# Performance work log

Measured on AMD Instinct MI355X. Metric: run time of the kernel, lower is better.

The kernel has to match this reference:

```python
import jax, jax.numpy as jnp
import numpy as np

C = 256
H = 8
D = C // H
B = 8
Q_PER = 128
KV_PER = 1024
NQ = B * Q_PER
NKV = B * KV_PER
NEG = -10000.0
MASK_EPS = 1e-6
RMS_EPS = float(np.finfo(np.float32).eps)  # torch RMSNorm default eps=None -> finfo eps


def _rms(x, w):
    return x * jax.lax.rsqrt(jnp.mean(x * x, axis=-1, keepdims=True) + RMS_EPS) * w


def _mlp(x, w1, b1, w2, b2):
    h = jax.nn.gelu(x @ w1.T + b1, approximate=False)  # torch nn.GELU is exact
    return h @ w2.T + b2


def _sdpa(qh, kh, vh, mask, scale):
    # qh [H, Nq, D], kh/vh [H, Nk, D], mask [Nq, Nk] additive
    s = jnp.einsum('hqd,hkd->hqk', qh, kh) * scale + mask[None]
    return jnp.einsum('hqk,hkd->hqd', jax.nn.softmax(s, axis=-1), vh)


def _heads(x):
    return x.reshape(-1, H, D).transpose(1, 0, 2)  # [H, N, D]


def setup_inputs() -> dict:
    key = jax.random.key(0)
    ks = jax.random.split(key, 24)
    s = 0.02
    lin = lambda k, o, i: jax.random.normal(k, (o, i), jnp.float32) * s
    inp = {
        'q': jax.random.normal(ks[0], (NQ, C), jnp.float32),
        'kv': jax.random.normal(ks[1], (NKV, C), jnp.float32),
        'cu_seqlens_q': jnp.arange(B + 1, dtype=jnp.int32) * Q_PER,
        'cu_seqlens_kv': jnp.arange(B + 1, dtype=jnp.int32) * KV_PER,
        'w_norm_kv': jnp.ones((C,), jnp.float32),
        'w_norm1': jnp.ones((C,), jnp.float32),
        'w_norm2': jnp.ones((C,), jnp.float32),
        'w_norm3': jnp.ones((C,), jnp.float32),
        'wq_c': lin(ks[2], C, C), 'wk_c': lin(ks[3], C, C), 'wv_c': lin(ks[4], C, C),
        'wo_c': lin(ks[5], C, C), 'bo_c': jnp.zeros((C,), jnp.float32),
        'wq_s': lin(ks[6], C, C), 'wkv_s': lin(ks[7], 2 * C, C),
        'wo_s': lin(ks[8], C, C), 'bo_s': jnp.zeros((C,), jnp.float32),
        'w1_mlp': lin(ks[9], 4 * C, C), 'b1_mlp': jnp.zeros((4 * C,), jnp.float32),
        'w2_mlp': lin(ks[10], C, 4 * C), 'b2_mlp': jnp.zeros((C,), jnp.float32),
        'w1_mask': lin(ks[11], C, C), 'b1_mask': jnp.zeros((C,), jnp.float32),
        'w2_mask': lin(ks[12], C, C), 'b2_mask': jnp.zeros((C,), jnp.float32),
    }
    return inp


def reference(q, kv, cu_seqlens_q, cu_seqlens_kv, w_norm_kv, w_norm1, w_norm2, w_norm3,
              wq_c, wk_c, wv_c, wo_c, bo_c, wq_s, wkv_s, wo_s, bo_s,
              w1_mlp, b1_mlp, w2_mlp, b2_mlp, w1_mask, b1_mask, w2_mask, b2_mask):
    scale = D ** (-0.5)
    nq, nkv = q.shape[0], kv.shape[0]
    # segment id per packed token from cu_seqlens
    seg_q = jnp.searchsorted(cu_seqlens_q, jnp.arange(nq), side='right') - 1
    seg_kv = jnp.searchsorted(cu_seqlens_kv, jnp.arange(nkv), side='right') - 1

    kv_n = _rms(kv, w_norm_kv)

    # mask MLP -> predicted attention mask (logits z), detached log-prob mask
    m_k = _mlp(q, w1_mask, b1_mask, w2_mask, b2_mask)          # [Nq, C]
    z = m_k @ kv_n.T                                           # [Nq, Nkv]
    p_hat = jax.nn.sigmoid(z)
    same = seg_q[:, None] == seg_kv[None, :]
    attn_mask = jnp.where(same, jnp.log(jax.lax.stop_gradient(p_hat) + MASK_EPS), NEG)

    # cross-attention (pre-norm)
    q_n = _rms(q, w_norm1)
    feat = _sdpa(_heads(q_n @ wq_c.T), _heads(kv_n @ wk_c.T), _heads(kv_n @ wv_c.T),
                 attn_mask, scale)
    feat = feat.transpose(1, 0, 2).reshape(-1, C) @ wo_c.T + bo_c
    q = q + feat

    # block-diagonal self-attention over queries
    q_n = _rms(q, w_norm2)
    kv_proj = (q_n @ wkv_s.T).reshape(-1, 2, H, D)
    self_mask = jnp.where(seg_q[:, None] == seg_q[None, :], 0.0, NEG)
    feat = _sdpa(_heads(q_n @ wq_s.T),
                 kv_proj[:, 0].transpose(1, 0, 2), kv_proj[:, 1].transpose(1, 0, 2),
                 self_mask, scale)
    feat = feat.transpose(1, 0, 2).reshape(-1, C) @ wo_s.T + bo_s
    q = q + feat

    # MLP
    q = q + _mlp(_rms(q, w_norm3), w1_mlp, b1_mlp, w2_mlp, b2_mlp)
    return q
```

## Files before the change

kernel.cpp:

```cpp
#include <hip/hip_runtime.h>
#include <math.h>


#define SCALE_ATTN 0.17677669529663687f
#define RMS_EPS 1.1920929e-07f

typedef __attribute__((ext_vector_type(8))) short bh8;
typedef __attribute__((ext_vector_type(4))) float f32x4;

__device__ __forceinline__ float bf2f(unsigned short s) {
  union { float f; unsigned u; } v; v.u = ((unsigned)s) << 16; return v.f;
}
__device__ __forceinline__ unsigned short f2bf(float f) {
  union { float f; unsigned u; } v; v.f = f;
  unsigned r = v.u + 0x7FFFu + ((v.u >> 16) & 1u);
  return (unsigned short)(r >> 16);
}
__device__ __forceinline__ unsigned pack2bf(float a, float b) {
  union { float f; unsigned u; } x, y; x.f = a; y.f = b;
  return ((x.u + 0x8000u) >> 16) | ((y.u + 0x8000u) & 0xFFFF0000u);
}
__device__ __forceinline__ float gelu_exact(float x) {
  return 0.5f * x * (1.0f + erff(x * 0.70710678118654752440f));
}
__device__ __forceinline__ float sum8sq(int4 v) {
  float s = 0.f;
  unsigned u[4] = {(unsigned)v.x, (unsigned)v.y, (unsigned)v.z, (unsigned)v.w};
#pragma unroll
  for (int i = 0; i < 4; ++i) {
    union { float f; unsigned q; } lo, hi;
    lo.q = u[i] << 16;
    hi.q = u[i] & 0xFFFF0000u;
    s += lo.f * lo.f + hi.f * hi.f;
  }
  return s;
}

struct WP { const float* p[12]; };
__global__ __launch_bounds__(256) void k_pre(
    WP wp, unsigned short* __restrict__ wbf, unsigned short* __restrict__ w2t,
    const float* __restrict__ wn1, const float* __restrict__ wn2,
    const float* __restrict__ wn3,
    const float* __restrict__ kv, const float* __restrict__ wnkv,
    const float* __restrict__ b2m, unsigned short* __restrict__ kv_n,
    float* __restrict__ tvec, unsigned short* __restrict__ q_n) {
  int bid = blockIdx.x, tid = threadIdx.x;
  if (bid < 1408) {
    long g = ((long)bid * 256 + tid) * 4;
    const float* src; long l;
    if (g < 327680)       { src = wp.p[g >> 16]; l = g & 65535; }
    else if (g < 458752)  { src = wp.p[5];  l = g - 327680; }
    else if (g < 524288)  { src = wp.p[6];  l = g - 458752; }
    else if (g < 786432)  { src = wp.p[7];  l = g - 524288; }
    else if (g < 1048576) { src = wp.p[8];  l = g - 786432; }
    else if (g < 1114112) { src = wp.p[9];  l = g - 1048576; }
    else if (g < 1179648) { src = wp.p[10]; l = g - 1114112; }
    else                  { src = wp.p[11]; l = g - 1179648; }
    float4 v = *(const float4*)(src + l);
    if (g >= 262144 && g < 458752) {
      int k = (int)(g & 255);
      v.x *= wn2[k]; v.y *= wn2[k + 1]; v.z *= wn2[k + 2]; v.w *= wn2[k + 3];
    } else if (g >= 524288 && g < 786432) {
      int k = (int)(g & 255);
      v.x *= wn3[k]; v.y *= wn3[k + 1]; v.z *= wn3[k + 2]; v.w *= wn3[k + 3];
    }
    ushort4 o;
    o.x = f2bf(v.x); o.y = f2bf(v.y); o.z = f2bf(v.z); o.w = f2bf(v.w);
    *(ushort4*)(wbf + g) = o;
  } else if (bid < 1424) {
    __shared__ float Ts[64][65];
    int t = bid - 1408, ti = t >> 2, tj = t & 3;
    const float* w2src = wp.p[10];
    int rr = tid >> 2;
#pragma unroll
    for (int j = 0; j < 4; ++j) {
      int cc = (tid & 3) * 16 + j * 4;
      float4 v = *(const float4*)(w2src + (long)(ti * 64 + rr) * 256 + tj * 64 + cc);
      Ts[rr][cc] = v.x; Ts[rr][cc + 1] = v.y;
      Ts[rr][cc + 2] = v.z; Ts[rr][cc + 3] = v.w;
    }
    __syncthreads();
#pragma unroll
    for (int j = 0; j < 4; ++j) {
      int kk = (tid & 3) * 16 + j * 4;
      ushort4 o;
      o.x = f2bf(Ts[kk][rr]); o.y = f2bf(Ts[kk + 1][rr]);
      o.z = f2bf(Ts[kk + 2][rr]); o.w = f2bf(Ts[kk + 3][rr]);
      *(ushort4*)(w2t + (long)(tj * 64 + rr) * 256 + ti * 64 + kk) = o;
    }
  } else if (bid < 3472) {
    int row = (bid - 1424) * 4 + (tid >> 6);
    int c4 = (tid & 63) * 4;
    float4 v = *(const float4*)(kv + (long)row * 256 + c4);
    float s = v.x * v.x + v.y * v.y + v.z * v.z + v.w * v.w;
#pragma unroll
    for (int off = 32; off > 0; off >>= 1) s += __shfl_xor(s, off, 64);
    float inv = rsqrtf(s * (1.0f / 256.0f) + RMS_EPS);
    float4 wn = *(const float4*)(wnkv + c4);
    float4 b2 = *(const float4*)(b2m + c4);
    float4 vn;
    vn.x = v.x * inv * wn.x; vn.y = v.y * inv * wn.y;
    vn.z = v.z * inv * wn.z; vn.w = v.w * inv * wn.w;
    ushort4 o;
    o.x = f2bf(vn.x); o.y = f2bf(vn.y); o.z = f2bf(vn.z); o.w = f2bf(vn.w);
    *(ushort4*)(kv_n + (long)row * 256 + c4) = o;
    float s2 = vn.x * b2.x + vn.y * b2.y + vn.z * b2.z + vn.w * b2.w;
#pragma unroll
    for (int off = 32; off > 0; off >>= 1) s2 += __shfl_xor(s2, off, 64);
    if ((tid & 63) == 0) tvec[row] = s2;
  } else {
    int row = (bid - 3472) * 4 + (tid >> 6);
    int c4 = (tid & 63) * 4;
    const float* q = wp.p[11];
    float4 v = *(const float4*)(q + (long)row * 256 + c4);
    float s = v.x * v.x + v.y * v.y + v.z * v.z + v.w * v.w;
#pragma unroll
    for (int off = 32; off > 0; off >>= 1) s += __shfl_xor(s, off, 64);
    float inv = rsqrtf(s * (1.0f / 256.0f) + RMS_EPS);
    float4 wn = *(const float4*)(wn1 + c4);
    ushort4 o;
    o.x = f2bf(v.x * inv * wn.x); o.y = f2bf(v.y * inv * wn.y);
    o.z = f2bf(v.z * inv * wn.z); o.w = f2bf(v.w * inv * wn.w);
    *(ushort4*)(q_n + (long)row * 256 + c4) = o;
  }
}

template <int MT, int KS, int EPI>
__device__ __forceinline__ void gemm_core(
    const unsigned short* __restrict__ A, const unsigned short* __restrict__ W,
    const float* bias, const float* R,
    float* Cf, unsigned short* Cb, unsigned short* Cb2,
    int lda, int ldw, int ldc, int m0, int n0) {
  int tid = threadIdx.x, w = tid >> 6, lane = tid & 63;
  int quad = lane >> 4, c = lane & 15;
  __shared__ __align__(16) unsigned short As[2][MT * 64][40];
  __shared__ __align__(16) unsigned short Ws[2][64][40];
  __shared__ float ssqLds[64];
  f32x4 acc[MT][4];
#pragma unroll
  for (int i = 0; i < MT; ++i)
#pragma unroll
    for (int j = 0; j < 4; ++j) acc[i][j] = (f32x4){0.f, 0.f, 0.f, 0.f};
  int ar = tid >> 2, ak = (tid & 3) * 8;
  float asum = 0.f;
  {
    int4 a0 = *(const int4*)(A + (long)(m0 + ar) * lda + ak);
    int4 a1;
    if (MT == 2) a1 = *(const int4*)(A + (long)(m0 + 64 + ar) * lda + ak);
    int4 wv = *(const int4*)(W + (long)(n0 + ar) * ldw + ak);
    if (EPI == 8) asum += sum8sq(a0);
    *(int4*)&As[0][ar][ak] = a0;
    if (MT == 2) *(int4*)&As[0][64 + ar][ak] = a1;
    *(int4*)&Ws[0][ar][ak] = wv;
  }
  __syncthreads();
#pragma unroll
  for (int i = 0; i < KS; ++i) {
    int cur = i & 1, nxt = cur ^ 1;
    int4 na0, na1, nwv;
    if (i + 1 < KS) {
      int k0 = (i + 1) * 32;
      na0 = *(const int4*)(A + (long)(m0 + ar) * lda + k0 + ak);
      if (MT == 2)
        na1 = *(const int4*)(A + (long)(m0 + 64 + ar) * lda + k0 + ak);
      nwv = *(const int4*)(W + (long)(n0 + ar) * ldw + k0 + ak);
    }
    bh8 af[MT];
#pragma unroll
    for (int mt = 0; mt < MT; ++mt)
      af[mt] = *(const bh8*)&As[cur][w * (16 * MT) + mt * 16 + c][quad * 8];
#pragma unroll
    for (int nt = 0; nt < 4; ++nt) {
      bh8 bf = *(const bh8*)&Ws[cur][nt * 16 + c][quad * 8];
#pragma unroll
      for (int mt = 0; mt < MT; ++mt)
        acc[mt][nt] =
            __builtin_amdgcn_mfma_f32_16x16x32_bf16(af[mt], bf, acc[mt][nt], 0, 0, 0);
    }
    if (i + 1 < KS) {
      if (EPI == 8) asum += sum8sq(na0);
      *(int4*)&As[nxt][ar][ak] = na0;
      if (MT == 2) *(int4*)&As[nxt][64 + ar][ak] = na1;
      *(int4*)&Ws[nxt][ar][ak] = nwv;
      __syncthreads();
    }
  }
  if (EPI == 8) {
    asum += __shfl_xor(asum, 1, 64);
    asum += __shfl_xor(asum, 2, 64);
    if ((tid & 3) == 0) ssqLds[ar] = asum;
    __syncthreads();
  }
#pragma unroll
  for (int mt = 0; mt < MT; ++mt)
#pragma unroll
    for (int nt = 0; nt < 4; ++nt)
#pragma unroll
      for (int r = 0; r < 4; ++r) {
        int lm = w * (16 * MT) + mt * 16 + quad * 4 + r;
        int m = m0 + lm;
        int n = n0 + nt * 16 + c;
        float v = acc[mt][nt][r];
        long ci = (long)m * ldc + n;
        if (EPI == 1) {
          if (bias) v += bias[n];
          Cb[ci] = f2bf(gelu_exact(v));
        } else if (EPI == 5) {
          Cb[ci] = f2bf(v);
        } else if (EPI == 2) {
          if (bias) v += bias[n];
          v += R[ci];
          Cf[ci] = v;
          if (Cb2) Cb2[ci] = f2bf(v);
        } else {
          v *= rsqrtf(ssqLds[lm] * (1.0f / 256.0f) + RMS_EPS);
          if (bias) v += bias[n];
          Cb[ci] = f2bf(gelu_exact(v));
        }
      }
}

template <int MT, int KS, int EPI>
__global__ __launch_bounds__(256) void k_gemm(
    const unsigned short* A, const unsigned short* W,
    const float* bias, const float* R,
    float* Cf, unsigned short* Cb, unsigned short* Cb2,
    int lda, int ldw, int ldc) {
  gemm_core<MT, KS, EPI>(A, W, bias, R, Cf, Cb, Cb2, lda, ldw, ldc,
                         blockIdx.y * (MT * 64), blockIdx.x * 64);
}

struct G4 {
  const unsigned short* A; const unsigned short* W;
  const float* bias; float* Cf; unsigned short* Cb;
  int lda, ldw, ldc, epi, nx, blkStart;
};
struct G4x { G4 g[4]; };
__global__ __launch_bounds__(256) void k_gemm4(G4x d) {
  int z = blockIdx.x;
  int i = 3;
  while (i > 0 && z < d.g[i].blkStart) --i;
  const G4& g = d.g[i];
  int local = z - g.blkStart;
  int by = local / g.nx, bx = local - by * g.nx;
  if (g.epi == 1)
    gemm_core<2, 8, 1>(g.A, g.W, g.bias, nullptr, nullptr, g.Cb, nullptr,
                       g.lda, g.ldw, g.ldc, by * 128, bx * 64);
  else
    gemm_core<2, 8, 5>(g.A, g.W, g.bias, nullptr, nullptr, g.Cb, nullptr,
                       g.lda, g.ldw, g.ldc, by * 128, bx * 64);
}

__global__ __launch_bounds__(256) void k_flash(
    const unsigned short* __restrict__ Qg,
    const unsigned short* __restrict__ KVg,
    const unsigned short* __restrict__ mh,
    const unsigned short* __restrict__ kvw,
    const float* __restrict__ tvec,
    float* __restrict__ partL, float* __restrict__ partO) {
  int split = blockIdx.x, bh = blockIdx.y;
  int b = bh >> 3, h = bh & 7, j0 = split * 128;
  int tid = threadIdx.x;
  int w = tid >> 6, lane = tid & 63, c = lane & 15, quad = lane >> 4;
  __shared__ __align__(16) unsigned short Ks[128][40];
  __shared__ __align__(16) unsigned short Vt[32][136];
  __shared__ __align__(16) unsigned short Pt[128][136];
  __shared__ float tvLds[128];
  const unsigned short* Qz = Qg + (long)(b * 128) * 256 + h * 32;
  const unsigned short* Kz = KVg + ((long)(b * 1024 + j0)) * 512 + h * 32;
  const unsigned short* Vz = Kz + 256;
  if (tid < 128) tvLds[tid] = tvec[b * 1024 + j0 + tid];
  bh8 Bq[2];
#pragma unroll
  for (int nt = 0; nt < 2; ++nt)
    Bq[nt] = *(const bh8*)(Qz + (long)(w * 32 + nt * 16 + c) * 256 + quad * 8);
  {
    int row = tid >> 2, part = tid & 3;
#pragma unroll
    for (int v = 0; v < 2; ++v) {
      int r2 = row + v * 64;
      *(int4*)&Ks[r2][part * 8] = *(const int4*)(Kz + (long)r2 * 512 + part * 8);
      int4 vv = *(const int4*)(Vz + (long)r2 * 512 + part * 8);
      unsigned short tmp[8];
      *(int4*)tmp = vv;
#pragma unroll
      for (int i = 0; i < 8; ++i) Vt[part * 8 + i][r2] = tmp[i];
    }
  }
  const unsigned short* Az = kvw + (long)(b * 1024 + j0) * 256;
  const unsigned short* Bz = mh + (long)(b * 128) * 256;
  f32x4 Z[8][2];
#pragma unroll
  for (int mt = 0; mt < 8; ++mt)
#pragma unroll
    for (int nt = 0; nt < 2; ++nt) Z[mt][nt] = (f32x4){0.f, 0.f, 0.f, 0.f};
#pragma unroll
  for (int k0 = 0; k0 < 256; k0 += 32) {
    bh8 bz[2];
#pragma unroll
    for (int nt = 0; nt < 2; ++nt)
      bz[nt] = *(const bh8*)(Bz + (long)(w * 32 + nt * 16 + c) * 256 + k0 + quad * 8);
#pragma unroll
    for (int mt = 0; mt < 8; ++mt) {
      bh8 az = *(const bh8*)(Az + (long)(mt * 16 + c) * 256 + k0 + quad * 8);
      Z[mt][0] = __builtin_amdgcn_mfma_f32_16x16x32_bf16(az, bz[0], Z[mt][0], 0, 0, 0);
      Z[mt][1] = __builtin_amdgcn_mfma_f32_16x16x32_bf16(az, bz[1], Z[mt][1], 0, 0, 0);
    }
  }
  __syncthreads();
  f32x4 S[8][2];
#pragma unroll
  for (int mt = 0; mt < 8; ++mt)
#pragma unroll
    for (int nt = 0; nt < 2; ++nt) S[mt][nt] = (f32x4){0.f, 0.f, 0.f, 0.f};
#pragma unroll
  for (int mt = 0; mt < 8; ++mt) {
    bh8 aK = *(const bh8*)&Ks[mt * 16 + c][quad * 8];
    S[mt][0] = __builtin_amdgcn_mfma_f32_16x16x32_bf16(aK, Bq[0], S[mt][0], 0, 0, 0);
    S[mt][1] = __builtin_amdgcn_mfma_f32_16x16x32_bf16(aK, Bq[1], S[mt][1], 0, 0, 0);
  }
  float L[2];
#pragma unroll
  for (int nt = 0; nt < 2; ++nt) {
    float rs = 0.f;
#pragma unroll
    for (int mt = 0; mt < 8; ++mt)
#pragma unroll
      for (int r = 0; r < 4; ++r) {
        float zz = Z[mt][nt][r] + tvLds[mt * 16 + quad * 4 + r];
        float p = 1.0f / (1.0f + __expf(-zz)) + 1e-6f;
        float e = __expf(S[mt][nt][r] * SCALE_ATTN) * p;
        S[mt][nt][r] = e;
        rs += e;
      }
    rs += __shfl_xor(rs, 16, 64);
    rs += __shfl_xor(rs, 32, 64);
    L[nt] = rs;
  }
#pragma unroll
  for (int mt = 0; mt < 8; ++mt)
#pragma unroll
    for (int nt = 0; nt < 2; ++nt) {
      uint2 pk;
      pk.x = pack2bf(S[mt][nt][0], S[mt][nt][1]);
      pk.y = pack2bf(S[mt][nt][2], S[mt][nt][3]);
      *(uint2*)&Pt[w * 32 + nt * 16 + c][mt * 16 + quad * 4] = pk;
    }
  __syncthreads();
  f32x4 acc[2][2];
#pragma unroll
  for (int i = 0; i < 2; ++i)
#pragma unroll
    for (int j = 0; j < 2; ++j) acc[i][j] = (f32x4){0.f, 0.f, 0.f, 0.f};
#pragma unroll
  for (int ks = 0; ks < 4; ++ks) {
    bh8 aP0 = *(const bh8*)&Pt[w * 32 + c][ks * 32 + quad * 8];
    bh8 aP1 = *(const bh8*)&Pt[w * 32 + 16 + c][ks * 32 + quad * 8];
    bh8 bV0 = *(const bh8*)&Vt[c][ks * 32 + quad * 8];
    bh8 bV1 = *(const bh8*)&Vt[16 + c][ks * 32 + quad * 8];
    acc[0][0] = __builtin_amdgcn_mfma_f32_16x16x32_bf16(aP0, bV0, acc[0][0], 0, 0, 0);
    acc[0][1] = __builtin_amdgcn_mfma_f32_16x16x32_bf16(aP0, bV1, acc[0][1], 0, 0, 0);
    acc[1][0] = __builtin_amdgcn_mfma_f32_16x16x32_bf16(aP1, bV0, acc[1][0], 0, 0, 0);
    acc[1][1] = __builtin_amdgcn_mfma_f32_16x16x32_bf16(aP1, bV1, acc[1][1], 0, 0, 0);
  }
  if (quad == 0) {
#pragma unroll
    for (int nt = 0; nt < 2; ++nt)
      partL[((long)(bh * 128 + w * 32 + nt * 16 + c)) * 8 + split] = L[nt];
  }
#pragma unroll
  for (int mt = 0; mt < 2; ++mt)
#pragma unroll
    for (int ct = 0; ct < 2; ++ct)
#pragma unroll
      for (int r = 0; r < 4; ++r) {
        int q = w * 32 + mt * 16 + quad * 4 + r;
        partO[(((long)(bh * 128 + q)) * 8 + split) * 32 + ct * 16 + c] =
            acc[mt][ct][r];
      }
}

__global__ __launch_bounds__(256) void k_gemm_cmb(
    const float* __restrict__ partL, const float* __restrict__ partO,
    const unsigned short* __restrict__ W, const float* __restrict__ bias,
    const float* __restrict__ R,
    float* __restrict__ Cf, unsigned short* __restrict__ Cb2) {
  int m0 = blockIdx.y * 64, n0 = blockIdx.x * 64;
  int tid = threadIdx.x, w = tid >> 6, lane = tid & 63;
  int quad = lane >> 4, c = lane & 15;
  __shared__ __align__(16) unsigned short As[2][64][40];
  __shared__ __align__(16) unsigned short Ws[2][64][40];
  __shared__ float Linv[64][8];
  int ar = tid >> 2, ak = (tid & 3) * 8;
  int b = m0 >> 7, q0 = m0 & 127;
  {
#pragma unroll
    for (int t = 0; t < 2; ++t) {
      int e = tid * 2 + t;
      int rr = e >> 3, hh = e & 7;
      const float* pl = partL + ((long)((b * 8 + hh) * 128 + q0 + rr)) * 8;
      float Ls = 0.f;
#pragma unroll
      for (int s = 0; s < 8; ++s) Ls += pl[s];
      Linv[rr][hh] = 1.0f / Ls;
    }
  }
  __syncthreads();
  auto computeA = [&](int i, uint4& pk) {
    const float* po =
        partO + (((long)((b * 8 + i) * 128 + q0 + ar)) * 8) * 32 + ak;
    float o0 = 0, o1 = 0, o2 = 0, o3 = 0, o4 = 0, o5 = 0, o6 = 0, o7 = 0;
#pragma unroll
    for (int s = 0; s < 8; ++s) {
      float4 u = *(const float4*)(po + s * 32);
      float4 v = *(const float4*)(po + s * 32 + 4);
      o0 += u.x; o1 += u.y; o2 += u.z; o3 += u.w;
      o4 += v.x; o5 += v.y; o6 += v.z; o7 += v.w;
    }
    float inv = Linv[ar][i];
    pk.x = pack2bf(o0 * inv, o1 * inv);
    pk.y = pack2bf(o2 * inv, o3 * inv);
    pk.z = pack2bf(o4 * inv, o5 * inv);
    pk.w = pack2bf(o6 * inv, o7 * inv);
  };
  f32x4 acc[4];
#pragma unroll
  for (int j = 0; j < 4; ++j) acc[j] = (f32x4){0.f, 0.f, 0.f, 0.f};
  {
    uint4 pk;
    computeA(0, pk);
    int4 wv = *(const int4*)(W + (long)(n0 + ar) * 256 + ak);
    *(uint4*)&As[0][ar][ak] = pk;
    *(int4*)&Ws[0][ar][ak] = wv;
  }
  __syncthreads();
#pragma unroll
  for (int i = 0; i < 8; ++i) {
    int cur = i & 1, nxt = cur ^ 1;
    uint4 npk;
    int4 nwv;
    if (i + 1 < 8) {
      computeA(i + 1, npk);
      nwv = *(const int4*)(W + (long)(n0 + ar) * 256 + (i + 1) * 32 + ak);
    }
    bh8 af = *(const bh8*)&As[cur][w * 16 + c][quad * 8];
#pragma unroll
    for (int nt = 0; nt < 4; ++nt) {
      bh8 bf = *(const bh8*)&Ws[cur][nt * 16 + c][quad * 8];
      acc[nt] = __builtin_amdgcn_mfma_f32_16x16x32_bf16(af, bf, acc[nt], 0, 0, 0);
    }
    if (i + 1 < 8) {
      *(uint4*)&As[nxt][ar][ak] = npk;
      *(int4*)&Ws[nxt][ar][ak] = nwv;
      __syncthreads();
    }
  }
#pragma unroll
  for (int nt = 0; nt < 4; ++nt)
#pragma unroll
    for (int r = 0; r < 4; ++r) {
      int m = m0 + w * 16 + quad * 4 + r;
      int n = n0 + nt * 16 + c;
      float v = acc[nt][r] + bias[n];
      long ci = (long)m * 256 + n;
      v += R[ci];
      Cf[ci] = v;
      Cb2[ci] = f2bf(v);
    }
}

__global__ __launch_bounds__(256) void k_selfattn(
    const unsigned short* __restrict__ X,
    const unsigned short* __restrict__ Wqkv,
    unsigned short* __restrict__ feat) {
  int z = blockIdx.x, b = z >> 3, h = z & 7;
  int tid = threadIdx.x, w = tid >> 6, lane = tid & 63;
  int c = lane & 15, quad = lane >> 4;
  __shared__ __align__(16) unsigned short Qs[128][40];
  __shared__ __align__(16) unsigned short Ks[128][40];
  __shared__ __align__(16) unsigned short Vt[32][136];
  __shared__ __align__(16) unsigned short Pt[128][136];
  __shared__ float ssqLds[128];
  const unsigned short* Xz = X + (long)(b * 128) * 256;
  int wr[6];
  wr[0] = h * 32;       wr[1] = h * 32 + 16;
  wr[2] = 256 + h * 32; wr[3] = 256 + h * 32 + 16;
  wr[4] = 512 + h * 32; wr[5] = 512 + h * 32 + 16;
  f32x4 acc[2][6];
#pragma unroll
  for (int i = 0; i < 2; ++i)
#pragma unroll
    for (int j = 0; j < 6; ++j) acc[i][j] = (f32x4){0.f, 0.f, 0.f, 0.f};
  float asq[2] = {0.f, 0.f};
#pragma unroll
  for (int k0 = 0; k0 < 256; k0 += 32) {
    bh8 af[2];
#pragma unroll
    for (int mt = 0; mt < 2; ++mt) {
      af[mt] = *(const bh8*)(Xz + (long)(w * 32 + mt * 16 + c) * 256 + k0 + quad * 8);
      asq[mt] += sum8sq(*(int4*)&af[mt]);
    }
#pragma unroll
    for (int nt = 0; nt < 6; ++nt) {
      bh8 wf = *(const bh8*)(Wqkv + (long)(wr[nt] + c) * 256 + k0 + quad * 8);
#pragma unroll
      for (int mt = 0; mt < 2; ++mt)
        acc[mt][nt] =
            __builtin_amdgcn_mfma_f32_16x16x32_bf16(af[mt], wf, acc[mt][nt], 0, 0, 0);
    }
  }
#pragma unroll
  for (int mt = 0; mt < 2; ++mt) {
    float s = asq[mt];
    s += __shfl_xor(s, 16, 64);
    s += __shfl_xor(s, 32, 64);
    if (quad == 0) ssqLds[w * 32 + mt * 16 + c] = s;
  }
#pragma unroll
  for (int mt = 0; mt < 2; ++mt)
#pragma unroll
    for (int r = 0; r < 4; ++r) {
      int tok = w * 32 + mt * 16 + quad * 4 + r;
      float inv = rsqrtf(ssqLds[tok] * (1.0f / 256.0f) + RMS_EPS);
#pragma unroll
      for (int nt = 0; nt < 6; ++nt) {
        unsigned short bv = f2bf(acc[mt][nt][r] * inv);
        if (nt < 2)      Qs[tok][nt * 16 + c] = bv;
        else if (nt < 4) Ks[tok][(nt - 2) * 16 + c] = bv;
        else             Vt[(nt - 4) * 16 + c][tok] = bv;
      }
    }
  __syncthreads();
  bh8 Bq[2];
#pragma unroll
  for (int nt = 0; nt < 2; ++nt)
    Bq[nt] = *(const bh8*)&Qs[w * 32 + nt * 16 + c][quad * 8];
  f32x4 S[8][2];
#pragma unroll
  for (int mt = 0; mt < 8; ++mt)
#pragma unroll
    for (int nt = 0; nt < 2; ++nt) S[mt][nt] = (f32x4){0.f, 0.f, 0.f, 0.f};
#pragma unroll
  for (int mt = 0; mt < 8; ++mt) {
    bh8 aK = *(const bh8*)&Ks[mt * 16 + c][quad * 8];
    S[mt][0] = __builtin_amdgcn_mfma_f32_16x16x32_bf16(aK, Bq[0], S[mt][0], 0, 0, 0);
    S[mt][1] = __builtin_amdgcn_mfma_f32_16x16x32_bf16(aK, Bq[1], S[mt][1], 0, 0, 0);
  }
  float L[2];
#pragma unroll
  for (int nt = 0; nt < 2; ++nt) {
    float rs = 0.f;
#pragma unroll
    for (int mt = 0; mt < 8; ++mt)
#pragma unroll
      for (int r = 0; r < 4; ++r) {
        float e = __expf(S[mt][nt][r] * SCALE_ATTN);
        S[mt][nt][r] = e;
        rs += e;
      }
    rs += __shfl_xor(rs, 16, 64);
    rs += __shfl_xor(rs, 32, 64);
    L[nt] = rs;
  }
#pragma unroll
  for (int mt = 0; mt < 8; ++mt)
#pragma unroll
    for (int nt = 0; nt < 2; ++nt) {
      uint2 pk;
      pk.x = pack2bf(S[mt][nt][0], S[mt][nt][1]);
      pk.y = pack2bf(S[mt][nt][2], S[mt][nt][3]);
      *(uint2*)&Pt[w * 32 + nt * 16 + c][mt * 16 + quad * 4] = pk;
    }
  __syncthreads();
  f32x4 o[2][2];
#pragma unroll
  for (int i = 0; i < 2; ++i)
#pragma unroll
    for (int j = 0; j < 2; ++j) o[i][j] = (f32x4){0.f, 0.f, 0.f, 0.f};
#pragma unroll
  for (int ks = 0; ks < 4; ++ks) {
    bh8 aP0 = *(const bh8*)&Pt[w * 32 + c][ks * 32 + quad * 8];
    bh8 aP1 = *(const bh8*)&Pt[w * 32 + 16 + c][ks * 32 + quad * 8];
    bh8 bV0 = *(const bh8*)&Vt[c][ks * 32 + quad * 8];
    bh8 bV1 = *(const bh8*)&Vt[16 + c][ks * 32 + quad * 8];
    o[0][0] = __builtin_amdgcn_mfma_f32_16x16x32_bf16(aP0, bV0, o[0][0], 0, 0, 0);
    o[0][1] = __builtin_amdgcn_mfma_f32_16x16x32_bf16(aP0, bV1, o[0][1], 0, 0, 0);
    o[1][0] = __builtin_amdgcn_mfma_f32_16x16x32_bf16(aP1, bV0, o[1][0], 0, 0, 0);
    o[1][1] = __builtin_amdgcn_mfma_f32_16x16x32_bf16(aP1, bV1, o[1][1], 0, 0, 0);
  }
  unsigned short* Oz = feat + (long)(b * 128) * 256 + h * 32;
#pragma unroll
  for (int mt = 0; mt < 2; ++mt)
#pragma unroll
    for (int r = 0; r < 4; ++r) {
      float linv = 1.0f / __shfl(L[mt], quad * 4 + r, 64);
      int q = w * 32 + mt * 16 + quad * 4 + r;
      Oz[(long)q * 256 + c] = f2bf(o[mt][0][r] * linv);
      Oz[(long)q * 256 + 16 + c] = f2bf(o[mt][1][r] * linv);
    }
}

extern "C" void kernel_launch(void* const* d_in, const int* in_sizes, int n_in,
                              void* d_out, int out_size, void* d_ws, size_t ws_size,
                              hipStream_t stream) {
  const float* q        = (const float*)d_in[0];
  const float* kv       = (const float*)d_in[1];
  const float* w_norm_kv = (const float*)d_in[4];
  const float* w_norm1  = (const float*)d_in[5];
  const float* w_norm2  = (const float*)d_in[6];
  const float* w_norm3  = (const float*)d_in[7];
  const float* bo_c     = (const float*)d_in[12];
  const float* bo_s     = (const float*)d_in[16];
  const float* b1_mlp   = (const float*)d_in[18];
  const float* b2_mlp   = (const float*)d_in[20];
  const float* b1_mask  = (const float*)d_in[22];
  const float* b2_mask  = (const float*)d_in[24];
  float* out = (float*)d_out;

  unsigned char* W8 = (unsigned char*)d_ws;
  unsigned short* wbf    = (unsigned short*)(W8 + 0);
  unsigned short* w2t    = (unsigned short*)(W8 + 2883584);
  unsigned short* kv_n   = (unsigned short*)(W8 + 3014656);
  unsigned short* q_n    = (unsigned short*)(W8 + 7208960);
  unsigned short* mh     = (unsigned short*)(W8 + 7733248);
  unsigned short* kvw    = (unsigned short*)(W8 + 8257536);
  float*          tvec   = (float*)(W8 + 14548992);
  unsigned short* Qc     = (unsigned short*)(W8 + 14581760);
  unsigned short* KVc    = (unsigned short*)(W8 + 15106048);
  unsigned short* feat   = (unsigned short*)(W8 + 25067520);
  unsigned short* out1_bf = (unsigned short*)(W8 + 25591808);
  unsigned short* out2_bf = (unsigned short*)(W8 + 26116096);
  float*          partL  = (float*)(W8 + 26648832);
  float*          partO  = (float*)(W8 + 26910976);
  unsigned short* hid    = (unsigned short*)(W8 + 35299584);

  unsigned short* wq_c_bf   = wbf;
  unsigned short* wkv_c_bf  = wbf + 65536;
  unsigned short* wo_c_bf   = wbf + 196608;
  unsigned short* wqkv_s_bf = wbf + 262144;
  unsigned short* wo_s_bf   = wbf + 458752;
  unsigned short* w1_mlp_bf = wbf + 524288;
  unsigned short* w2_mlp_bf = wbf + 786432;
  unsigned short* w1_mask_bf = wbf + 1048576;
  unsigned short* q_bf      = wbf + 1179648;

  WP wp;
  wp.p[0] = (const float*)d_in[8];  wp.p[1] = (const float*)d_in[9];
  wp.p[2] = (const float*)d_in[10]; wp.p[3] = (const float*)d_in[11];
  wp.p[4] = (const float*)d_in[13]; wp.p[5] = (const float*)d_in[14];
  wp.p[6] = (const float*)d_in[15]; wp.p[7] = (const float*)d_in[17];
  wp.p[8] = (const float*)d_in[19]; wp.p[9] = (const float*)d_in[21];
  wp.p[10] = (const float*)d_in[23]; wp.p[11] = q;
  k_pre<<<3728, 256, 0, stream>>>(wp, wbf, w2t, w_norm1, w_norm2, w_norm3,
                                  kv, w_norm_kv, b2_mask, kv_n, tvec, q_n);

  G4x d;
  d.g[0] = {q_bf, w1_mask_bf, b1_mask, nullptr, mh, 256, 256, 256, 1, 4, 0};
  d.g[1] = {q_n, wq_c_bf, nullptr, nullptr, Qc, 256, 256, 256, 5, 4, 32};
  d.g[2] = {kv_n, wkv_c_bf, nullptr, nullptr, KVc, 256, 256, 512, 5, 8, 64};
  d.g[3] = {kv_n, w2t, nullptr, nullptr, kvw, 256, 256, 256, 5, 4, 576};
  k_gemm4<<<832, 256, 0, stream>>>(d);

  k_flash<<<dim3(8, 64), 256, 0, stream>>>(Qc, KVc, mh, kvw, tvec,
                                           partL, partO);

  k_gemm_cmb<<<dim3(4, 16), 256, 0, stream>>>(partL, partO, wo_c_bf, bo_c, q,
                                              out, out1_bf);

  k_selfattn<<<64, 256, 0, stream>>>(out1_bf, wqkv_s_bf, feat);

  k_gemm<1, 8, 2><<<dim3(4, 16), 256, 0, stream>>>(
      feat, wo_s_bf, bo_s, out, out, nullptr, out2_bf, 256, 256, 256);

  k_gemm<1, 8, 8><<<dim3(16, 16), 256, 0, stream>>>(
      out2_bf, w1_mlp_bf, b1_mlp, nullptr, nullptr, hid, nullptr, 256, 256, 1024);

  k_gemm<1, 32, 2><<<dim3(4, 16), 256, 0, stream>>>(
      hid, w2_mlp_bf, b2_mlp, out, out, nullptr, nullptr, 1024, 1024, 256);
}
```

Measured before the change: 215.4 us.

## Fuse all stages into one cooperative persistent megakernel with grid syncs

Replaces the chain of separate kernel launches with a single cooperative kernel. A persistent grid loops over work items for each stage, and stages are separated by grid.sync, with shared memory overlaid through a union. The mask logits are split out of the flash kernel into their own GEMM stage that writes a bf16 sigmoid mask, which flash then reads. The aim is to remove launch gaps and inter-kernel overhead, at the cost of grid-sync latency, an extra mask buffer round trip through memory, and possible occupancy limits from the union shared memory. A fallback path launches the separate kernels if the cooperative launch fails.

```diff
diff --git a/kernel.cpp b/kernel.cpp
--- a/kernel.cpp
+++ b/kernel.cpp
@@ -1,5 +1,8 @@
 #include <hip/hip_runtime.h>
+#include <hip/hip_cooperative_groups.h>
 #include <math.h>
+
+namespace cg = cooperative_groups;
 
 
 #define SCALE_ATTN 0.17677669529663687f
@@ -36,106 +39,122 @@
   return s;
 }
 
-struct WP { const float* p[12]; };
-__global__ __launch_bounds__(256) void k_pre(
-    WP wp, unsigned short* __restrict__ wbf, unsigned short* __restrict__ w2t,
-    const float* __restrict__ wn1, const float* __restrict__ wn2,
-    const float* __restrict__ wn3,
-    const float* __restrict__ kv, const float* __restrict__ wnkv,
-    const float* __restrict__ b2m, unsigned short* __restrict__ kv_n,
-    float* __restrict__ tvec, unsigned short* __restrict__ q_n) {
-  int bid = blockIdx.x, tid = threadIdx.x;
-  if (bid < 1408) {
-    long g = ((long)bid * 256 + tid) * 4;
+union SMem {
+  struct { float Ts[64][65]; } pre;
+  struct { unsigned short As[2][128][40]; unsigned short Ws[2][64][40];
+           float ssq[64]; } gm;
+  struct { unsigned short Ks[128][40]; unsigned short Vt[32][136];
+           unsigned short Pt[128][136]; } fl;
+  struct { unsigned short Qs[128][40]; unsigned short Ks[128][40];
+           unsigned short Vt[32][136]; unsigned short Pt[128][136];
+           float ssq[128]; } sa;
+  struct { unsigned short As[2][64][40]; unsigned short Ws[2][64][40];
+           float Linv[64][8]; } cm;
+};
+
+struct KArgs {
+  const float* p[12];
+  const float *wn1, *wn2, *wn3, *wnkv, *kv;
+  const float *bo_c, *bo_s, *b1_mlp, *b2_mlp, *b1_mask, *b2_mask;
+  unsigned short *wbf, *w2t, *kv_n, *q_n, *mh, *kvw, *maskp, *Qc, *KVc,
+                 *feat, *out1, *out2, *hid;
+  float *tvec, *partL, *partO, *out;
+  const unsigned short *wq_c, *wkv_c, *wo_c, *wqkv_s, *wo_s, *w1m, *w2m,
+                       *w1mask, *qbf;
+};
+
+__device__ void pre_item(int item, int tid, SMem& sm, const KArgs& A) {
+  if (item < 1408) {
+    long g = ((long)item * 256 + tid) * 4;
     const float* src; long l;
-    if (g < 327680)       { src = wp.p[g >> 16]; l = g & 65535; }
-    else if (g < 458752)  { src = wp.p[5];  l = g - 327680; }
-    else if (g < 524288)  { src = wp.p[6];  l = g - 458752; }
-    else if (g < 786432)  { src = wp.p[7];  l = g - 524288; }
-    else if (g < 1048576) { src = wp.p[8];  l = g - 786432; }
-    else if (g < 1114112) { src = wp.p[9];  l = g - 1048576; }
-    else if (g < 1179648) { src = wp.p[10]; l = g - 1114112; }
-    else                  { src = wp.p[11]; l = g - 1179648; }
+    if (g < 327680)       { src = A.p[g >> 16]; l = g & 65535; }
+    else if (g < 458752)  { src = A.p[5];  l = g - 327680; }
+    else if (g < 524288)  { src = A.p[6];  l = g - 458752; }
+    else if (g < 786432)  { src = A.p[7];  l = g - 524288; }
+    else if (g < 1048576) { src = A.p[8];  l = g - 786432; }
+    else if (g < 1114112) { src = A.p[9];  l = g - 1048576; }
+    else if (g < 1179648) { src = A.p[10]; l = g - 1114112; }
+    else                  { src = A.p[11]; l = g - 1179648; }
     float4 v = *(const float4*)(src + l);
     if (g >= 262144 && g < 458752) {
       int k = (int)(g & 255);
-      v.x *= wn2[k]; v.y *= wn2[k + 1]; v.z *= wn2[k + 2]; v.w *= wn2[k + 3];
+      v.x *= A.wn2[k]; v.y *= A.wn2[k + 1];
+      v.z *= A.wn2[k + 2]; v.w *= A.wn2[k + 3];
     } else if (g >= 524288 && g < 786432) {
       int k = (int)(g & 255);
-      v.x *= wn3[k]; v.y *= wn3[k + 1]; v.z *= wn3[k + 2]; v.w *= wn3[k + 3];
+      v.x *= A.wn3[k]; v.y *= A.wn3[k + 1];
+      v.z *= A.wn3[k + 2]; v.w *= A.wn3[k + 3];
     }
     ushort4 o;
     o.x = f2bf(v.x); o.y = f2bf(v.y); o.z = f2bf(v.z); o.w = f2bf(v.w);
-    *(ushort4*)(wbf + g) = o;
-  } else if (bid < 1424) {
-    __shared__ float Ts[64][65];
-    int t = bid - 1408, ti = t >> 2, tj = t & 3;
-    const float* w2src = wp.p[10];
+    *(ushort4*)(A.wbf + g) = o;
+  } else if (item < 1424) {
+    int t = item - 1408, ti = t >> 2, tj = t & 3;
+    const float* w2src = A.p[10];
     int rr = tid >> 2;
 #pragma unroll
     for (int j = 0; j < 4; ++j) {
       int cc = (tid & 3) * 16 + j * 4;
       float4 v = *(const float4*)(w2src + (long)(ti * 64 + rr) * 256 + tj * 64 + cc);
-      Ts[rr][cc] = v.x; Ts[rr][cc + 1] = v.y;
-      Ts[rr][cc + 2] = v.z; Ts[rr][cc + 3] = v.w;
+      sm.pre.Ts[rr][cc] = v.x; sm.pre.Ts[rr][cc + 1] = v.y;
+      sm.pre.Ts[rr][cc + 2] = v.z; sm.pre.Ts[rr][cc + 3] = v.w;
     }
     __syncthreads();
 #pragma unroll
     for (int j = 0; j < 4; ++j) {
       int kk = (tid & 3) * 16 + j * 4;
       ushort4 o;
-      o.x = f2bf(Ts[kk][rr]); o.y = f2bf(Ts[kk + 1][rr]);
-      o.z = f2bf(Ts[kk + 2][rr]); o.w = f2bf(Ts[kk + 3][rr]);
-      *(ushort4*)(w2t + (long)(tj * 64 + rr) * 256 + ti * 64 + kk) = o;
-    }
-  } else if (bid < 3472) {
-    int row = (bid - 1424) * 4 + (tid >> 6);
+      o.x = f2bf(sm.pre.Ts[kk][rr]); o.y = f2bf(sm.pre.Ts[kk + 1][rr]);
+      o.z = f2bf(sm.pre.Ts[kk + 2][rr]); o.w = f2bf(sm.pre.Ts[kk + 3][rr]);
+      *(ushort4*)(A.w2t + (long)(tj * 64 + rr) * 256 + ti * 64 + kk) = o;
+    }
+  } else if (item < 3472) {
+    int row = (item - 1424) * 4 + (tid >> 6);
     int c4 = (tid & 63) * 4;
-    float4 v = *(const float4*)(kv + (long)row * 256 + c4);
+    float4 v = *(const float4*)(A.kv + (long)row * 256 + c4);
     float s = v.x * v.x + v.y * v.y + v.z * v.z + v.w * v.w;
 #pragma unroll
     for (int off = 32; off > 0; off >>= 1) s += __shfl_xor(s, off, 64);
     float inv = rsqrtf(s * (1.0f / 256.0f) + RMS_EPS);
-    float4 wn = *(const float4*)(wnkv + c4);
-    float4 b2 = *(const float4*)(b2m + c4);
+    float4 wn = *(const float4*)(A.wnkv + c4);
+    float4 b2 = *(const float4*)(A.b2_mask + c4);
     float4 vn;
     vn.x = v.x * inv * wn.x; vn.y = v.y * inv * wn.y;
     vn.z = v.z * inv * wn.z; vn.w = v.w * inv * wn.w;
     ushort4 o;
     o.x = f2bf(vn.x); o.y = f2bf(vn.y); o.z = f2bf(vn.z); o.w = f2bf(vn.w);
-    *(ushort4*)(kv_n + (long)row * 256 + c4) = o;
+    *(ushort4*)(A.kv_n + (long)row * 256 + c4) = o;
     float s2 = vn.x * b2.x + vn.y * b2.y + vn.z * b2.z + vn.w * b2.w;
 #pragma unroll
     for (int off = 32; off > 0; off >>= 1) s2 += __shfl_xor(s2, off, 64);
-    if ((tid & 63) == 0) tvec[row] = s2;
+    if ((tid & 63) == 0) A.tvec[row] = s2;
   } else {
-    int row = (bid - 3472) * 4 + (tid >> 6);
+    int row = (item - 3472) * 4 + (tid >> 6);
     int c4 = (tid & 63) * 4;
-    const float* q = wp.p[11];
+    const float* q = A.p[11];
     float4 v = *(const float4*)(q + (long)row * 256 + c4);
     float s = v.x * v.x + v.y * v.y + v.z * v.z + v.w * v.w;
 #pragma unroll
     for (int off = 32; off > 0; off >>= 1) s += __shfl_xor(s, off, 64);
     float inv = rsqrtf(s * (1.0f / 256.0f) + RMS_EPS);
-    float4 wn = *(const float4*)(wn1 + c4);
+    float4 wn = *(const float4*)(A.wn1 + c4);
     ushort4 o;
     o.x = f2bf(v.x * inv * wn.x); o.y = f2bf(v.y * inv * wn.y);
     o.z = f2bf(v.z * inv * wn.z); o.w = f2bf(v.w * inv * wn.w);
-    *(ushort4*)(q_n + (long)row * 256 + c4) = o;
+    *(ushort4*)(A.q_n + (long)row * 256 + c4) = o;
   }
 }
 
 template <int MT, int KS, int EPI>
-__device__ __forceinline__ void gemm_core(
-    const unsigned short* __restrict__ A, const unsigned short* __restrict__ W,
+__device__ __forceinline__ void gemm_core(SMem& sm,
+    const unsigned short* __restrict__ Ain, const unsigned short* __restrict__ W,
     const float* bias, const float* R,
     float* Cf, unsigned short* Cb, unsigned short* Cb2,
     int lda, int ldw, int ldc, int m0, int n0) {
   int tid = threadIdx.x, w = tid >> 6, lane = tid & 63;
   int quad = lane >> 4, c = lane & 15;
-  __shared__ __align__(16) unsigned short As[2][MT * 64][40];
-  __shared__ __align__(16) unsigned short Ws[2][64][40];
-  __shared__ float ssqLds[64];
+  auto& As = sm.gm.As;
+  auto& Ws = sm.gm.Ws;
   f32x4 acc[MT][4];
 #pragma unroll
   for (int i = 0; i < MT; ++i)
@@ -144,9 +163,9 @@
   int ar = tid >> 2, ak = (tid & 3) * 8;
   float asum = 0.f;
   {
-    int4 a0 = *(const int4*)(A + (long)(m0 + ar) * lda + ak);
+    int4 a0 = *(const int4*)(Ain + (long)(m0 + ar) * lda + ak);
     int4 a1;
-    if (MT == 2) a1 = *(const int4*)(A + (long)(m0 + 64 + ar) * lda + ak);
+    if (MT == 2) a1 = *(const int4*)(Ain + (long)(m0 + 64 + ar) * lda + ak);
     int4 wv = *(const int4*)(W + (long)(n0 + ar) * ldw + ak);
     if (EPI == 8) asum += sum8sq(a0);
     *(int4*)&As[0][ar][ak] = a0;
@@ -160,9 +179,9 @@
     int4 na0, na1, nwv;
     if (i + 1 < KS) {
       int k0 = (i + 1) * 32;
-      na0 = *(const int4*)(A + (long)(m0 + ar) * lda + k0 + ak);
+      na0 = *(const int4*)(Ain + (long)(m0 + ar) * lda + k0 + ak);
       if (MT == 2)
-        na1 = *(const int4*)(A + (long)(m0 + 64 + ar) * lda + k0 + ak);
+        na1 = *(const int4*)(Ain + (long)(m0 + 64 + ar) * lda + k0 + ak);
       nwv = *(const int4*)(W + (long)(n0 + ar) * ldw + k0 + ak);
     }
     bh8 af[MT];
@@ -188,7 +207,7 @@
   if (EPI == 8) {
     asum += __shfl_xor(asum, 1, 64);
     asum += __shfl_xor(asum, 2, 64);
-    if ((tid & 3) == 0) ssqLds[ar] = asum;
+    if ((tid & 3) == 0) sm.gm.ssq[ar] = asum;
     __syncthreads();
   }
 #pragma unroll
@@ -207,69 +226,63 @@
           Cb[ci] = f2bf(gelu_exact(v));
         } else if (EPI == 5) {
           Cb[ci] = f2bf(v);
+        } else if (EPI == 3) {
+          v += bias[n];
+          Cb[ci] = f2bf(1.0f / (1.0f + __expf(-v)) + 1e-6f);
         } else if (EPI == 2) {
           if (bias) v += bias[n];
           v += R[ci];
           Cf[ci] = v;
           if (Cb2) Cb2[ci] = f2bf(v);
         } else {
-          v *= rsqrtf(ssqLds[lm] * (1.0f / 256.0f) + RMS_EPS);
+          v *= rsqrtf(sm.gm.ssq[lm] * (1.0f / 256.0f) + RMS_EPS);
           if (bias) v += bias[n];
           Cb[ci] = f2bf(gelu_exact(v));
         }
       }
 }
 
-template <int MT, int KS, int EPI>
-__global__ __launch_bounds__(256) void k_gemm(
-    const unsigned short* A, const unsigned short* W,
-    const float* bias, const float* R,
-    float* Cf, unsigned short* Cb, unsigned short* Cb2,
-    int lda, int ldw, int ldc) {
-  gemm_core<MT, KS, EPI>(A, W, bias, R, Cf, Cb, Cb2, lda, ldw, ldc,
-                         blockIdx.y * (MT * 64), blockIdx.x * 64);
-}
-
-struct G4 {
-  const unsigned short* A; const unsigned short* W;
-  const float* bias; float* Cf; unsigned short* Cb;
-  int lda, ldw, ldc, epi, nx, blkStart;
-};
-struct G4x { G4 g[4]; };
-__global__ __launch_bounds__(256) void k_gemm4(G4x d) {
-  int z = blockIdx.x;
-  int i = 3;
-  while (i > 0 && z < d.g[i].blkStart) --i;
-  const G4& g = d.g[i];
-  int local = z - g.blkStart;
-  int by = local / g.nx, bx = local - by * g.nx;
-  if (g.epi == 1)
-    gemm_core<2, 8, 1>(g.A, g.W, g.bias, nullptr, nullptr, g.Cb, nullptr,
-                       g.lda, g.ldw, g.ldc, by * 128, bx * 64);
-  else
-    gemm_core<2, 8, 5>(g.A, g.W, g.bias, nullptr, nullptr, g.Cb, nullptr,
-                       g.lda, g.ldw, g.ldc, by * 128, bx * 64);
-}
-
-__global__ __launch_bounds__(256) void k_flash(
-    const unsigned short* __restrict__ Qg,
-    const unsigned short* __restrict__ KVg,
-    const unsigned short* __restrict__ mh,
-    const unsigned short* __restrict__ kvw,
-    const float* __restrict__ tvec,
-    float* __restrict__ partL, float* __restrict__ partO) {
-  int split = blockIdx.x, bh = blockIdx.y;
+__device__ void stage2_item(int item, SMem& sm, const KArgs& A) {
+  if (item < 32) {
+    int l = item;
+    gemm_core<2, 8, 1>(sm, A.qbf, A.w1mask, A.b1_mask, nullptr,
+                       nullptr, A.mh, nullptr, 256, 256, 256,
+                       (l >> 2) * 128, (l & 3) * 64);
+  } else if (item < 64) {
+    int l = item - 32;
+    gemm_core<2, 8, 5>(sm, A.q_n, A.wq_c, nullptr, nullptr,
+                       nullptr, A.Qc, nullptr, 256, 256, 256,
+                       (l >> 2) * 128, (l & 3) * 64);
+  } else if (item < 576) {
+    int l = item - 64;
+    gemm_core<2, 8, 5>(sm, A.kv_n, A.wkv_c, nullptr, nullptr,
+                       nullptr, A.KVc, nullptr, 256, 256, 512,
+                       (l >> 3) * 128, (l & 7) * 64);
+  } else {
+    int l = item - 576;
+    gemm_core<2, 8, 5>(sm, A.kv_n, A.w2t, nullptr, nullptr,
+                       nullptr, A.kvw, nullptr, 256, 256, 256,
+                       (l >> 2) * 128, (l & 3) * 64);
+  }
+}
+__device__ void mask_item(int item, SMem& sm, const KArgs& A) {
+  int z = item >> 5, r = item & 31;
+  gemm_core<1, 8, 3>(sm, A.mh + (long)z * 128 * 256,
+                     A.kvw + (long)z * 1024 * 256, A.tvec + (long)z * 1024,
+                     nullptr, nullptr, A.maskp + (long)z * 128 * 1024,
+                     nullptr, 256, 256, 1024, (r >> 4) * 64, (r & 15) * 64);
+}
+
+__device__ void flash_item(int item, int tid, SMem& sm, const KArgs& A) {
+  int split = item & 7, bh = item >> 3;
   int b = bh >> 3, h = bh & 7, j0 = split * 128;
-  int tid = threadIdx.x;
   int w = tid >> 6, lane = tid & 63, c = lane & 15, quad = lane >> 4;
-  __shared__ __align__(16) unsigned short Ks[128][40];
-  __shared__ __align__(16) unsigned short Vt[32][136];
-  __shared__ __align__(16) unsigned short Pt[128][136];
-  __shared__ float tvLds[128];
-  const unsigned short* Qz = Qg + (long)(b * 128) * 256 + h * 32;
-  const unsigned short* Kz = KVg + ((long)(b * 1024 + j0)) * 512 + h * 32;
+  auto& Ks = sm.fl.Ks;
+  auto& Vt = sm.fl.Vt;
+  auto& Pt = sm.fl.Pt;
+  const unsigned short* Qz = A.Qc + (long)(b * 128) * 256 + h * 32;
+  const unsigned short* Kz = A.KVc + ((long)(b * 1024 + j0)) * 512 + h * 32;
   const unsigned short* Vz = Kz + 256;
-  if (tid < 128) tvLds[tid] = tvec[b * 1024 + j0 + tid];
   bh8 Bq[2];
 #pragma unroll
   for (int nt = 0; nt < 2; ++nt)
@@ -287,26 +300,6 @@
       for (int i = 0; i < 8; ++i) Vt[part * 8 + i][r2] = tmp[i];
     }
   }
-  const unsigned short* Az = kvw + (long)(b * 1024 + j0) * 256;
-  const unsigned short* Bz = mh + (long)(b * 128) * 256;
-  f32x4 Z[8][2];
-#pragma unroll
-  for (int mt = 0; mt < 8; ++mt)
-#pragma unroll
-    for (int nt = 0; nt < 2; ++nt) Z[mt][nt] = (f32x4){0.f, 0.f, 0.f, 0.f};
-#pragma unroll
-  for (int k0 = 0; k0 < 256; k0 += 32) {
-    bh8 bz[2];
-#pragma unroll
-    for (int nt = 0; nt < 2; ++nt)
-      bz[nt] = *(const bh8*)(Bz + (long)(w * 32 + nt * 16 + c) * 256 + k0 + quad * 8);
-#pragma unroll
-    for (int mt = 0; mt < 8; ++mt) {
-      bh8 az = *(const bh8*)(Az + (long)(mt * 16 + c) * 256 + k0 + quad * 8);
-      Z[mt][0] = __builtin_amdgcn_mfma_f32_16x16x32_bf16(az, bz[0], Z[mt][0], 0, 0, 0);
-      Z[mt][1] = __builtin_amdgcn_mfma_f32_16x16x32_bf16(az, bz[1], Z[mt][1], 0, 0, 0);
-    }
-  }
   __syncthreads();
   f32x4 S[8][2];
 #pragma unroll
@@ -322,17 +315,21 @@
   float L[2];
 #pragma unroll
   for (int nt = 0; nt < 2; ++nt) {
+    const unsigned short* mrow =
+        A.maskp + ((long)(b * 128 + w * 32 + nt * 16 + c)) * 1024 + j0;
+#pragma unroll
+    for (int mt = 0; mt < 8; ++mt) {
+      uint2 mp = *(const uint2*)(mrow + mt * 16 + quad * 4);
+      S[mt][nt][0] = __expf(S[mt][nt][0] * SCALE_ATTN) * bf2f((unsigned short)mp.x);
+      S[mt][nt][1] = __expf(S[mt][nt][1] * SCALE_ATTN) * bf2f((unsigned short)(mp.x >> 16));
+      S[mt][nt][2] = __expf(S[mt][nt][2] * SCALE_ATTN) * bf2f((unsigned short)mp.y);
+      S[mt][nt][3] = __expf(S[mt][nt][3] * SCALE_ATTN) * bf2f((unsigned short)(mp.y >> 16));
+    }
     float rs = 0.f;
 #pragma unroll
     for (int mt = 0; mt < 8; ++mt)
 #pragma unroll
-      for (int r = 0; r < 4; ++r) {
-        float zz = Z[mt][nt][r] + tvLds[mt * 16 + quad * 4 + r];
-        float p = 1.0f / (1.0f + __expf(-zz)) + 1e-6f;
-        float e = __expf(S[mt][nt][r] * SCALE_ATTN) * p;
-        S[mt][nt][r] = e;
-        rs += e;
-      }
+      for (int r = 0; r < 4; ++r) rs += S[mt][nt][r];
     rs += __shfl_xor(rs, 16, 64);
     rs += __shfl_xor(rs, 32, 64);
     L[nt] = rs;
@@ -366,7 +363,7 @@
   if (quad == 0) {
 #pragma unroll
     for (int nt = 0; nt < 2; ++nt)
-      partL[((long)(bh * 128 + w * 32 + nt * 16 + c)) * 8 + split] = L[nt];
+      A.partL[((long)(bh * 128 + w * 32 + nt * 16 + c)) * 8 + split] = L[nt];
   }
 #pragma unroll
   for (int mt = 0; mt < 2; ++mt)
@@ -375,40 +372,34 @@
 #pragma unroll
       for (int r = 0; r < 4; ++r) {
         int q = w * 32 + mt * 16 + quad * 4 + r;
-        partO[(((long)(bh * 128 + q)) * 8 + split) * 32 + ct * 16 + c] =
+        A.partO[(((long)(bh * 128 + q)) * 8 + split) * 32 + ct * 16 + c] =
             acc[mt][ct][r];
       }
 }
 
-__global__ __launch_bounds__(256) void k_gemm_cmb(
-    const float* __restrict__ partL, const float* __restrict__ partO,
-    const unsigned short* __restrict__ W, const float* __restrict__ bias,
-    const float* __restrict__ R,
-    float* __restrict__ Cf, unsigned short* __restrict__ Cb2) {
-  int m0 = blockIdx.y * 64, n0 = blockIdx.x * 64;
-  int tid = threadIdx.x, w = tid >> 6, lane = tid & 63;
+__device__ void cmb_item(int item, int tid, SMem& sm, const KArgs& A) {
+  int m0 = (item >> 2) * 64, n0 = (item & 3) * 64;
+  int w = tid >> 6, lane = tid & 63;
   int quad = lane >> 4, c = lane & 15;
-  __shared__ __align__(16) unsigned short As[2][64][40];
-  __shared__ __align__(16) unsigned short Ws[2][64][40];
-  __shared__ float Linv[64][8];
+  auto& As = sm.cm.As;
+  auto& Ws = sm.cm.Ws;
+  auto& Linv = sm.cm.Linv;
   int ar = tid >> 2, ak = (tid & 3) * 8;
   int b = m0 >> 7, q0 = m0 & 127;
-  {
-#pragma unroll
-    for (int t = 0; t < 2; ++t) {
-      int e = tid * 2 + t;
-      int rr = e >> 3, hh = e & 7;
-      const float* pl = partL + ((long)((b * 8 + hh) * 128 + q0 + rr)) * 8;
-      float Ls = 0.f;
-#pragma unroll
-      for (int s = 0; s < 8; ++s) Ls += pl[s];
-      Linv[rr][hh] = 1.0f / Ls;
-    }
+#pragma unroll
+  for (int t = 0; t < 2; ++t) {
+    int e = tid * 2 + t;
+    int rr = e >> 3, hh = e & 7;
+    const float* pl = A.partL + ((long)((b * 8 + hh) * 128 + q0 + rr)) * 8;
+    float Ls = 0.f;
+#pragma unroll
+    for (int s = 0; s < 8; ++s) Ls += pl[s];
+    Linv[rr][hh] = 1.0f / Ls;
   }
   __syncthreads();
   auto computeA = [&](int i, uint4& pk) {
     const float* po =
-        partO + (((long)((b * 8 + i) * 128 + q0 + ar)) * 8) * 32 + ak;
+        A.partO + (((long)((b * 8 + i) * 128 + q0 + ar)) * 8) * 32 + ak;
     float o0 = 0, o1 = 0, o2 = 0, o3 = 0, o4 = 0, o5 = 0, o6 = 0, o7 = 0;
 #pragma unroll
     for (int s = 0; s < 8; ++s) {
@@ -429,7 +420,7 @@
   {
     uint4 pk;
     computeA(0, pk);
-    int4 wv = *(const int4*)(W + (long)(n0 + ar) * 256 + ak);
+    int4 wv = *(const int4*)(A.wo_c + (long)(n0 + ar) * 256 + ak);
     *(uint4*)&As[0][ar][ak] = pk;
     *(int4*)&Ws[0][ar][ak] = wv;
   }
@@ -441,7 +432,7 @@
     int4 nwv;
     if (i + 1 < 8) {
       computeA(i + 1, npk);
-      nwv = *(const int4*)(W + (long)(n0 + ar) * 256 + (i + 1) * 32 + ak);
+      nwv = *(const int4*)(A.wo_c + (long)(n0 + ar) * 256 + (i + 1) * 32 + ak);
     }
     bh8 af = *(const bh8*)&As[cur][w * 16 + c][quad * 8];
 #pragma unroll
@@ -461,27 +452,24 @@
     for (int r = 0; r < 4; ++r) {
       int m = m0 + w * 16 + quad * 4 + r;
       int n = n0 + nt * 16 + c;
-      float v = acc[nt][r] + bias[n];
+      float v = acc[nt][r] + A.bo_c[n];
       long ci = (long)m * 256 + n;
-      v += R[ci];
-      Cf[ci] = v;
-      Cb2[ci] = f2bf(v);
-    }
-}
-
-__global__ __launch_bounds__(256) void k_selfattn(
-    const unsigned short* __restrict__ X,
-    const unsigned short* __restrict__ Wqkv,
-    unsigned short* __restrict__ feat) {
-  int z = blockIdx.x, b = z >> 3, h = z & 7;
-  int tid = threadIdx.x, w = tid >> 6, lane = tid & 63;
+      v += A.p[11][ci];
+      A.out[ci] = v;
+      A.out1[ci] = f2bf(v);
+    }
+}
+
+__device__ void selfattn_item(int item, int tid, SMem& sm, const KArgs& A) {
+  int b = item >> 3, h = item & 7;
+  int w = tid >> 6, lane = tid & 63;
   int c = lane & 15, quad = lane >> 4;
-  __shared__ __align__(16) unsigned short Qs[128][40];
-  __shared__ __align__(16) unsigned short Ks[128][40];
-  __shared__ __align__(16) unsigned short Vt[32][136];
-  __shared__ __align__(16) unsigned short Pt[128][136];
-  __shared__ float ssqLds[128];
-  const unsigned short* Xz = X + (long)(b * 128) * 256;
+  auto& Qs = sm.sa.Qs;
+  auto& Ks = sm.sa.Ks;
+  auto& Vt = sm.sa.Vt;
+  auto& Pt = sm.sa.Pt;
+  auto& ssqLds = sm.sa.ssq;
+  const unsigned short* Xz = A.out1 + (long)(b * 128) * 256;
   int wr[6];
   wr[0] = h * 32;       wr[1] = h * 32 + 16;
   wr[2] = 256 + h * 32; wr[3] = 256 + h * 32 + 16;
@@ -502,7 +490,7 @@
     }
 #pragma unroll
     for (int nt = 0; nt < 6; ++nt) {
-      bh8 wf = *(const bh8*)(Wqkv + (long)(wr[nt] + c) * 256 + k0 + quad * 8);
+      bh8 wf = *(const bh8*)(A.wqkv_s + (long)(wr[nt] + c) * 256 + k0 + quad * 8);
 #pragma unroll
       for (int mt = 0; mt < 2; ++mt)
         acc[mt][nt] =
@@ -588,7 +576,7 @@
     o[1][0] = __builtin_amdgcn_mfma_f32_16x16x32_bf16(aP1, bV0, o[1][0], 0, 0, 0);
     o[1][1] = __builtin_amdgcn_mfma_f32_16x16x32_bf16(aP1, bV1, o[1][1], 0, 0, 0);
   }
-  unsigned short* Oz = feat + (long)(b * 128) * 256 + h * 32;
+  unsigned short* Oz = A.feat + (long)(b * 128) * 256 + h * 32;
 #pragma unroll
   for (int mt = 0; mt < 2; ++mt)
 #pragma unroll
@@ -600,81 +588,173 @@
     }
 }
 
+__device__ void wos_item(int item, SMem& sm, const KArgs& A) {
+  gemm_core<1, 8, 2>(sm, A.feat, A.wo_s, A.bo_s, A.out, A.out, nullptr,
+                     A.out2, 256, 256, 256, (item >> 2) * 64, (item & 3) * 64);
+}
+__device__ void mlp1_item(int item, SMem& sm, const KArgs& A) {
+  gemm_core<1, 8, 8>(sm, A.out2, A.w1m, A.b1_mlp, nullptr, nullptr, A.hid,
+                     nullptr, 256, 256, 1024, (item >> 4) * 64, (item & 15) * 64);
+}
+__device__ void mlp2_item(int item, SMem& sm, const KArgs& A) {
+  gemm_core<1, 32, 2>(sm, A.hid, A.w2m, A.b2_mlp, A.out, A.out, nullptr,
+                      nullptr, 1024, 1024, 256, (item >> 2) * 64, (item & 3) * 64);
+}
+
+#define GRIDN 256
+__global__ __launch_bounds__(256) void k_mega(KArgs A) {
+  __shared__ SMem sm;
+  int bid = blockIdx.x, tid = threadIdx.x;
+  cg::grid_group grid = cg::this_grid();
+
+  for (int item = bid; item < 3728; item += GRIDN) {
+    __syncthreads();
+    pre_item(item, tid, sm, A);
+  }
+  grid.sync();
+  for (int item = bid; item < 832; item += GRIDN) {
+    __syncthreads();
+    stage2_item(item, sm, A);
+  }
+  grid.sync();
+  for (int item = bid; item < 256; item += GRIDN) {
+    __syncthreads();
+    mask_item(item, sm, A);
+  }
+  grid.sync();
+  for (int item = bid; item < 512; item += GRIDN) {
+    __syncthreads();
+    flash_item(item, tid, sm, A);
+  }
+  grid.sync();
+  for (int item = bid; item < 64; item += GRIDN) {
+    __syncthreads();
+    cmb_item(item, tid, sm, A);
+  }
+  grid.sync();
+  for (int item = bid; item < 64; item += GRIDN) {
+    __syncthreads();
+    selfattn_item(item, tid, sm, A);
+  }
+  grid.sync();
+  for (int item = bid; item < 64; item += GRIDN) {
+    __syncthreads();
+    wos_item(item, sm, A);
+  }
+  grid.sync();
+  for (int item = bid; item < 256; item += GRIDN) {
+    __syncthreads();
+    mlp1_item(item, sm, A);
+  }
+  grid.sync();
+  for (int item = bid; item < 64; item += GRIDN) {
+    __syncthreads();
+    mlp2_item(item, sm, A);
+  }
+}
+
+__global__ __launch_bounds__(256) void g_pre(KArgs A) {
+  __shared__ SMem sm;
+  pre_item(blockIdx.x, threadIdx.x, sm, A);
+}
+__global__ __launch_bounds__(256) void g_stage2(KArgs A) {
+  __shared__ SMem sm;
+  stage2_item(blockIdx.x, sm, A);
+}
+__global__ __launch_bounds__(256) void g_mask(KArgs A) {
+  __shared__ SMem sm;
+  mask_item(blockIdx.x, sm, A);
+}
+__global__ __launch_bounds__(256) void g_flash(KArgs A) {
+  __shared__ SMem sm;
+  flash_item(blockIdx.x, threadIdx.x, sm, A);
+}
+__global__ __launch_bounds__(256) void g_cmb(KArgs A) {
+  __shared__ SMem sm;
+  cmb_item(blockIdx.x, threadIdx.x, sm, A);
+}
+__global__ __launch_bounds__(256) void g_selfattn(KArgs A) {
+  __shared__ SMem sm;
+  selfattn_item(blockIdx.x, threadIdx.x, sm, A);
+}
+__global__ __launch_bounds__(256) void g_wos(KArgs A) {
+  __shared__ SMem sm;
+  wos_item(blockIdx.x, sm, A);
+}
+__global__ __launch_bounds__(256) void g_mlp1(KArgs A) {
+  __shared__ SMem sm;
+  mlp1_item(blockIdx.x, sm, A);
+}
+__global__ __launch_bounds__(256) void g_mlp2(KArgs A) {
+  __shared__ SMem sm;
+  mlp2_item(blockIdx.x, sm, A);
+}
+
 extern "C" void kernel_launch(void* const* d_in, const int* in_sizes, int n_in,
                               void* d_out, int out_size, void* d_ws, size_t ws_size,
                               hipStream_t stream) {
-  const float* q        = (const float*)d_in[0];
-  const float* kv       = (const float*)d_in[1];
-  const float* w_norm_kv = (const float*)d_in[4];
-  const float* w_norm1  = (const float*)d_in[5];
-  const float* w_norm2  = (const float*)d_in[6];
-  const float* w_norm3  = (const float*)d_in[7];
-  const float* bo_c     = (const float*)d_in[12];
-  const float* bo_s     = (const float*)d_in[16];
-  const float* b1_mlp   = (const float*)d_in[18];
-  const float* b2_mlp   = (const float*)d_in[20];
-  const float* b1_mask  = (const float*)d_in[22];
-  const float* b2_mask  = (const float*)d_in[24];
-  float* out = (float*)d_out;
-
   unsigned char* W8 = (unsigned char*)d_ws;
-  unsigned short* wbf    = (unsigned short*)(W8 + 0);
-  unsigned short* w2t    = (unsigned short*)(W8 + 2883584);
-  unsigned short* kv_n   = (unsigned short*)(W8 + 3014656);
-  unsigned short* q_n    = (unsigned short*)(W8 + 7208960);
-  unsigned short* mh     = (unsigned short*)(W8 + 7733248);
-  unsigned short* kvw    = (unsigned short*)(W8 + 8257536);
-  float*          tvec   = (float*)(W8 + 14548992);
-  unsigned short* Qc     = (unsigned short*)(W8 + 14581760);
-  unsigned short* KVc    = (unsigned short*)(W8 + 15106048);
-  unsigned short* feat   = (unsigned short*)(W8 + 25067520);
-  unsigned short* out1_bf = (unsigned short*)(W8 + 25591808);
-  unsigned short* out2_bf = (unsigned short*)(W8 + 26116096);
-  float*          partL  = (float*)(W8 + 26648832);
-  float*          partO  = (float*)(W8 + 26910976);
-  unsigned short* hid    = (unsigned short*)(W8 + 35299584);
-
-  unsigned short* wq_c_bf   = wbf;
-  unsigned short* wkv_c_bf  = wbf + 65536;
-  unsigned short* wo_c_bf   = wbf + 196608;
-  unsigned short* wqkv_s_bf = wbf + 262144;
-  unsigned short* wo_s_bf   = wbf + 458752;
-  unsigned short* w1_mlp_bf = wbf + 524288;
-  unsigned short* w2_mlp_bf = wbf + 786432;
-  unsigned short* w1_mask_bf = wbf + 1048576;
-  unsigned short* q_bf      = wbf + 1179648;
-
-  WP wp;
-  wp.p[0] = (const float*)d_in[8];  wp.p[1] = (const float*)d_in[9];
-  wp.p[2] = (const float*)d_in[10]; wp.p[3] = (const float*)d_in[11];
-  wp.p[4] = (const float*)d_in[13]; wp.p[5] = (const float*)d_in[14];
-  wp.p[6] = (const float*)d_in[15]; wp.p[7] = (const float*)d_in[17];
-  wp.p[8] = (const float*)d_in[19]; wp.p[9] = (const float*)d_in[21];
-  wp.p[10] = (const float*)d_in[23]; wp.p[11] = q;
-  k_pre<<<3728, 256, 0, stream>>>(wp, wbf, w2t, w_norm1, w_norm2, w_norm3,
-                                  kv, w_norm_kv, b2_mask, kv_n, tvec, q_n);
-
-  G4x d;
-  d.g[0] = {q_bf, w1_mask_bf, b1_mask, nullptr, mh, 256, 256, 256, 1, 4, 0};
-  d.g[1] = {q_n, wq_c_bf, nullptr, nullptr, Qc, 256, 256, 256, 5, 4, 32};
-  d.g[2] = {kv_n, wkv_c_bf, nullptr, nullptr, KVc, 256, 256, 512, 5, 8, 64};
-  d.g[3] = {kv_n, w2t, nullptr, nullptr, kvw, 256, 256, 256, 5, 4, 576};
-  k_gemm4<<<832, 256, 0, stream>>>(d);
-
-  k_flash<<<dim3(8, 64), 256, 0, stream>>>(Qc, KVc, mh, kvw, tvec,
-                                           partL, partO);
-
-  k_gemm_cmb<<<dim3(4, 16), 256, 0, stream>>>(partL, partO, wo_c_bf, bo_c, q,
-                                              out, out1_bf);
-
-  k_selfattn<<<64, 256, 0, stream>>>(out1_bf, wqkv_s_bf, feat);
-
-  k_gemm<1, 8, 2><<<dim3(4, 16), 256, 0, stream>>>(
-      feat, wo_s_bf, bo_s, out, out, nullptr, out2_bf, 256, 256, 256);
-
-  k_gemm<1, 8, 8><<<dim3(16, 16), 256, 0, stream>>>(
-      out2_bf, w1_mlp_bf, b1_mlp, nullptr, nullptr, hid, nullptr, 256, 256, 1024);
-
-  k_gemm<1, 32, 2><<<dim3(4, 16), 256, 0, stream>>>(
-      hid, w2_mlp_bf, b2_mlp, out, out, nullptr, nullptr, 1024, 1024, 256);
-}
+  KArgs ka;
+  ka.p[0] = (const float*)d_in[8];   ka.p[1] = (const float*)d_in[9];
+  ka.p[2] = (const float*)d_in[10];  ka.p[3] = (const float*)d_in[11];
+  ka.p[4] = (const float*)d_in[13];  ka.p[5] = (const float*)d_in[14];
+  ka.p[6] = (const float*)d_in[15];  ka.p[7] = (const float*)d_in[17];
+  ka.p[8] = (const float*)d_in[19];  ka.p[9] = (const float*)d_in[21];
+  ka.p[10] = (const float*)d_in[23]; ka.p[11] = (const float*)d_in[0];
+  ka.wn1 = (const float*)d_in[5];
+  ka.wn2 = (const float*)d_in[6];
+  ka.wn3 = (const float*)d_in[7];
+  ka.wnkv = (const float*)d_in[4];
+  ka.kv = (const float*)d_in[1];
+  ka.bo_c = (const float*)d_in[12];
+  ka.bo_s = (const float*)d_in[16];
+  ka.b1_mlp = (const float*)d_in[18];
+  ka.b2_mlp = (const float*)d_in[20];
+  ka.b1_mask = (const float*)d_in[22];
+  ka.b2_mask = (const float*)d_in[24];
+
+  unsigned short* wbf = (unsigned short*)(W8 + 0);
+  ka.wbf   = wbf;
+  ka.w2t   = (unsigned short*)(W8 + 2883584);
+  ka.kv_n  = (unsigned short*)(W8 + 3014656);
+  ka.q_n   = (unsigned short*)(W8 + 7208960);
+  ka.mh    = (unsigned short*)(W8 + 7733248);
+  ka.kvw   = (unsigned short*)(W8 + 8257536);
+  ka.maskp = (unsigned short*)(W8 + 12451840);
+  ka.tvec  = (float*)(W8 + 14548992);
+  ka.Qc    = (unsigned short*)(W8 + 14581760);
+  ka.KVc   = (unsigned short*)(W8 + 15106048);
+  ka.feat  = (unsigned short*)(W8 + 25067520);
+  ka.out1  = (unsigned short*)(W8 + 25591808);
+  ka.out2  = (unsigned short*)(W8 + 26116096);
+  ka.partL = (float*)(W8 + 26648832);
+  ka.partO = (float*)(W8 + 26910976);
+  ka.hid   = (unsigned short*)(W8 + 35299584);
+  ka.out   = (float*)d_out;
+
+  ka.wq_c   = wbf;
+  ka.wkv_c  = wbf + 65536;
+  ka.wo_c   = wbf + 196608;
+  ka.wqkv_s = wbf + 262144;
+  ka.wo_s   = wbf + 458752;
+  ka.w1m    = wbf + 524288;
+  ka.w2m    = wbf + 786432;
+  ka.w1mask = wbf + 1048576;
+  ka.qbf    = wbf + 1179648;
+
+  void* kparams[] = {&ka};
+  hipError_t err = hipLaunchCooperativeKernel(
+      (const void*)k_mega, dim3(GRIDN, 1, 1), dim3(256, 1, 1), kparams, 0,
+      stream);
+  if (err != hipSuccess) {
+    g_pre<<<3728, 256, 0, stream>>>(ka);
+    g_stage2<<<832, 256, 0, stream>>>(ka);
+    g_mask<<<256, 256, 0, stream>>>(ka);
+    g_flash<<<512, 256, 0, stream>>>(ka);
+    g_cmb<<<64, 256, 0, stream>>>(ka);
+    g_selfattn<<<64, 256, 0, stream>>>(ka);
+    g_wos<<<64, 256, 0, stream>>>(ka);
+    g_mlp1<<<256, 256, 0, stream>>>(ka);
+    g_mlp2<<<64, 256, 0, stream>>>(ka);
+  }
+}
```

Result: slower. 477.3 us (+121.6%).
